# Performance work log

Measured on AMD Instinct MI355X. Metric: run time of the kernel, lower is better.

Reference implementation:

```python
import jax, jax.numpy as jnp
import numpy as np

B, L, F, P = 128, 256, 4, 4   # dialogs, dialog length, future/past links
IN, H, C = 1024, 256, 7
N = B * L


def _build_edges():
    # same structure as build_intra_graph: self-loop + F future + P past per node
    i = np.arange(L)
    ss, tt = [], []
    for d in range(-P, F + 1):
        j = i + d
        m = (j >= 0) & (j < L)
        ss.append(i[m]); tt.append(j[m])
    s = np.concatenate(ss); t = np.concatenate(tt)
    offs = (np.arange(B) * L)[:, None]
    S = (s[None, :] + offs).ravel()
    T = (t[None, :] + offs).ravel()
    return np.stack([S, T]).astype(np.int32)


def setup_inputs() -> dict:
    key = jax.random.key(0)
    ks = jax.random.split(key, 16)
    ei = _build_edges()
    speakers = np.asarray(jax.random.randint(ks[0], (N,), 0, 2), dtype=np.int32)
    rel = (speakers[ei[0]] * speakers[ei[1]]).astype(np.int32)
    sd_in = 1.0 / np.sqrt(IN)
    sd_h = 1.0 / np.sqrt(H)
    return {
        "input": jax.random.normal(ks[1], (N, IN), jnp.float32),
        "dialog_lengths": jnp.full((B,), L, jnp.int32),
        "speakers": jnp.asarray(speakers),
        "labels": jax.random.randint(ks[2], (N,), 0, C, jnp.int32),
        "edge_index": jnp.asarray(ei),
        "rel_type": jnp.asarray(rel),
        # RGCNConv(IN, H, num_relations=2): per-relation weight, root weight, bias
        "W_rgcn": jax.random.normal(ks[3], (2, IN, H), jnp.float32) * sd_in,
        "W_root": jax.random.normal(ks[4], (IN, H), jnp.float32) * sd_in,
        "b_rgcn": jax.random.normal(ks[5], (H,), jnp.float32) * 0.01,
        # GraphConv(H, H): lin_rel (on aggregated neighbors, with bias), lin_root (no bias)
        "W_rel": jax.random.normal(ks[6], (H, H), jnp.float32) * sd_h,
        "b_rel": jax.random.normal(ks[7], (H,), jnp.float32) * 0.01,
        "W_grt": jax.random.normal(ks[8], (H, H), jnp.float32) * sd_h,
        # skip_con: Linear(IN, H)
        "W_skip": jax.random.normal(ks[9], (IN, H), jnp.float32) * sd_in,
        "b_skip": jax.random.normal(ks[10], (H,), jnp.float32) * 0.01,
        # classify: Linear(H, C)
        "W_cls": jax.random.normal(ks[11], (H, C), jnp.float32) * sd_h,
        "b_cls": jax.random.normal(ks[12], (C,), jnp.float32) * 0.01,
    }


def reference(input, dialog_lengths, speakers, labels, edge_index, rel_type,
              W_rgcn, W_root, b_rgcn, W_rel, b_rel, W_grt,
              W_skip, b_skip, W_cls, b_cls):
    n = input.shape[0]
    src, dst = edge_index[0], edge_index[1]
    seg = jax.ops.segment_sum

    # --- RGCNConv: out_i = x_i @ W_root + b + sum_r mean_{j in N_r(i)} x_j @ W_r
    t = jnp.einsum('ni,rio->rno', input, W_rgcn)      # [2, N, H]
    msg = t[rel_type, src]                            # [E, H] relation-specific messages
    h = input @ W_root + b_rgcn
    for r in range(2):
        m = (rel_type == r).astype(input.dtype)       # [E]
        s = seg(msg * m[:, None], dst, num_segments=n)
        cnt = seg(m, dst, num_segments=n)
        h = h + s / jnp.maximum(cnt, 1.0)[:, None]    # mean aggregation per relation

    # --- GraphConv (aggr='add'): out_i = W_rel @ sum_j h_j + b_rel + W_grt @ h_i
    neigh = seg(h[src], dst, num_segments=n)          # [N, H]
    h2 = neigh @ W_rel + b_rel + h @ W_grt

    # --- skip connection + classifier
    out = (h2 + input @ W_skip + b_skip) @ W_cls + b_cls  # [N, C]

    # --- cross entropy (mean)
    logp = jax.nn.log_softmax(out, axis=-1)
    loss = -jnp.mean(jnp.take_along_axis(logp, labels[:, None].astype(jnp.int32), axis=1))
    return out, loss
```

## Files before the change

### kernel.cpp

```cpp
#include <hip/hip_runtime.h>

#define NN 32768
#define INF 1024
#define HF 256

typedef __bf16 bf16x8 __attribute__((ext_vector_type(8)));
typedef float f32x4 __attribute__((ext_vector_type(4)));
typedef unsigned short u16x8 __attribute__((ext_vector_type(8)));

__device__ __forceinline__ float bf2f(unsigned short u) {
  union { unsigned int i; float f; } v; v.i = ((unsigned int)u) << 16; return v.f;
}
__device__ __forceinline__ unsigned short f2bf(float f) {
  union { float f; unsigned int i; } v; v.f = f;
  unsigned int x = v.i;
  return (unsigned short)((x + 0x7fffu + ((x >> 16) & 1u)) >> 16);
}

__device__ __forceinline__ void ld_lds16(const unsigned short* g, unsigned short* l) {
  __builtin_amdgcn_global_load_lds(
      (__attribute__((address_space(1))) const unsigned int*)g,
      (__attribute__((address_space(3))) unsigned int*)l, 16, 0, 0);
}

__global__ __launch_bounds__(256)
void diagcn_prep(const float* __restrict__ x, const float* __restrict__ Wrgcn,
                 const float* __restrict__ Wroot, const float* __restrict__ Wskip,
                 const float* __restrict__ Wgrt, const float* __restrict__ Wrel,
                 unsigned short* __restrict__ Xbf, unsigned short* __restrict__ WbigT,
                 unsigned short* __restrict__ WsmT, float* __restrict__ loss) {
  int bid = blockIdx.x;
  if (bid < 32768) {
    if (bid == 0 && threadIdx.x == 0) loss[0] = 0.f;
    int idx = bid * 256 + threadIdx.x;
    float4 v = ((const float4*)x)[idx];
    ushort4 u; u.x = f2bf(v.x); u.y = f2bf(v.y); u.z = f2bf(v.z); u.w = f2bf(v.w);
    ((ushort4*)Xbf)[idx] = u;
    return;
  }
  __shared__ float tile[64 * 65];
  int tb = bid - 32768;
  const float* src;
  int k0, ncol0;
  unsigned short* dst;
  int ldd, nrow0;
  if (tb < 256) {
    int tn = tb >> 4, tk = tb & 15;
    int mat = tn >> 2;
    src = (mat == 0) ? Wrgcn : (mat == 1) ? (Wrgcn + 262144) : (mat == 2) ? Wroot : Wskip;
    k0 = tk * 64; ncol0 = (tn & 3) * 64;
    dst = WbigT; ldd = 1024; nrow0 = tn * 64;
  } else {
    int t2 = tb - 256;
    int tn = t2 >> 3, tk = t2 & 7;
    src = (tk < 4) ? Wgrt : Wrel;
    k0 = (tk & 3) * 64; ncol0 = tn * 64;
    dst = WsmT; ldd = 512; nrow0 = tn * 64;
  }
  int kdst0 = (tb < 256) ? k0 : (((tb - 256) & 7) * 64);
  int c = threadIdx.x & 63, rb = threadIdx.x >> 6;
#pragma unroll
  for (int it = 0; it < 16; ++it) {
    int r = rb + it * 4;
    tile[r * 65 + c] = src[(size_t)(k0 + r) * 256 + ncol0 + c];
  }
  __syncthreads();
  int kk = threadIdx.x & 63;
#pragma unroll
  for (int it = 0; it < 16; ++it) {
    int nn = rb + it * 4;
    dst[(size_t)(nrow0 + nn) * ldd + kdst0 + kk] = f2bf(tile[kk * 65 + nn]);
  }
}

__global__ __launch_bounds__(256)
void diagcn_gemm1(const unsigned short* __restrict__ A, const unsigned short* __restrict__ BT,
                  unsigned short* __restrict__ Y) {
  const int K = 1024;
  __shared__ unsigned short As[128 * 64];
  __shared__ unsigned short Bs[128 * 64];
  const int tid = threadIdx.x;
  const int w = tid >> 6, lane = tid & 63;
  const int wm = w >> 1, wn = w & 1;
  const int quad = lane >> 4, l15 = lane & 15;
  const int b = blockIdx.x;
  const int m0 = (((b & 7) << 5) + (b >> 6)) << 7;
  const int n0 = ((b >> 3) & 7) << 7;
  const int rowg = lane >> 3;
  const int kbsw = (lane & 7) ^ rowg;

  f32x4 acc[4][4] = {};
  const unsigned short* Abase = A + (size_t)m0 * K + kbsw * 8;
  const unsigned short* Bbase = BT + (size_t)n0 * K + kbsw * 8;

  for (int k0 = 0; k0 < K; k0 += 64) {
#pragma unroll
    for (int t = 0; t < 4; ++t) {
      int grp = w * 4 + t;
      int rl = grp * 8 + rowg;
      ld_lds16(Abase + (size_t)rl * K + k0, &As[grp * 512]);
      ld_lds16(Bbase + (size_t)rl * K + k0, &Bs[grp * 512]);
    }
    __syncthreads();
#pragma unroll
    for (int ks = 0; ks < 2; ++ks) {
      bf16x8 av[4], bv[4];
      int kb = ks * 4 + quad;
#pragma unroll
      for (int i = 0; i < 4; ++i) {
        int ra = wm * 64 + i * 16 + l15;
        int rb2 = wn * 64 + i * 16 + l15;
        av[i] = *(const bf16x8*)&As[ra * 64 + ((kb ^ (ra & 7)) << 3)];
        bv[i] = *(const bf16x8*)&Bs[rb2 * 64 + ((kb ^ (rb2 & 7)) << 3)];
      }
#pragma unroll
      for (int i = 0; i < 4; ++i)
#pragma unroll
        for (int j = 0; j < 4; ++j)
          acc[i][j] = __builtin_amdgcn_mfma_f32_16x16x32_bf16(av[i], bv[j], acc[i][j], 0, 0, 0);
    }
    __syncthreads();
  }
#pragma unroll
  for (int i = 0; i < 4; ++i)
#pragma unroll
    for (int j = 0; j < 4; ++j) {
      int row = m0 + wm * 64 + i * 16 + quad * 4;
      int col = n0 + wn * 64 + j * 16 + l15;
#pragma unroll
      for (int r = 0; r < 4; ++r)
        Y[(size_t)(row + r) * 1024 + col] = f2bf(acc[i][j][r]);
    }
}

__global__ __launch_bounds__(256)
void diagcn_h(const unsigned short* __restrict__ Y, const int* __restrict__ spk,
              const float* __restrict__ brgcn, unsigned short* __restrict__ A2) {
  int b = blockIdx.x;
  int wv = threadIdx.x >> 6, lane = threadIdx.x & 63;
  int half = lane >> 5, li = lane & 31, c0 = li << 3;
  int node = ((b & 7) << 12) + ((b >> 3) << 3) + wv * 2 + half;
  int p = node & 255, dbase = node - p;
  int si = spk[node];
  float a0[8] = {}, a1[8] = {};
  float n0 = 0.f, n1 = 0.f;
#pragma unroll
  for (int d = -4; d <= 4; ++d) {
    int pj = p + d;
    float w = (pj >= 0 && pj < 256) ? 1.f : 0.f;
    int jc = pj < 0 ? 0 : (pj > 255 ? 255 : pj);
    int nj = dbase + jc;
    int rel = si & spk[nj];
    u16x8 v = *(const u16x8*)&Y[(size_t)nj * 1024 + (rel << 8) + c0];
    float w1 = rel ? w : 0.f, w0 = rel ? 0.f : w;
#pragma unroll
    for (int k = 0; k < 8; ++k) {
      float f = bf2f(v[k]);
      a0[k] += f * w0; a1[k] += f * w1;
    }
    n0 += w0; n1 += w1;
  }
  u16x8 vr = *(const u16x8*)&Y[(size_t)node * 1024 + 512 + c0];
  float i0 = 1.f / fmaxf(n0, 1.f), i1 = 1.f / fmaxf(n1, 1.f);
  u16x8 u;
#pragma unroll
  for (int k = 0; k < 8; ++k)
    u[k] = f2bf(bf2f(vr[k]) + brgcn[c0 + k] + a0[k] * i0 + a1[k] * i1);
  *(u16x8*)&A2[(size_t)node * 512 + c0] = u;
}

__global__ __launch_bounds__(256)
void diagcn_neigh(unsigned short* __restrict__ A2) {
  int b = blockIdx.x;
  int wv = threadIdx.x >> 6, lane = threadIdx.x & 63;
  int half = lane >> 5, li = lane & 31, c0 = li << 3;
  int node = ((b & 7) << 12) + ((b >> 3) << 3) + wv * 2 + half;
  int p = node & 255, dbase = node - p;
  float s[8] = {};
#pragma unroll
  for (int d = -4; d <= 4; ++d) {
    int pj = p + d;
    float w = (pj >= 0 && pj < 256) ? 1.f : 0.f;
    int jc = pj < 0 ? 0 : (pj > 255 ? 255 : pj);
    u16x8 v = *(const u16x8*)&A2[(size_t)(dbase + jc) * 512 + c0];
#pragma unroll
    for (int k = 0; k < 8; ++k) s[k] += bf2f(v[k]) * w;
  }
  u16x8 u;
#pragma unroll
  for (int k = 0; k < 8; ++k) u[k] = f2bf(s[k]);
  *(u16x8*)&A2[(size_t)node * 512 + 256 + c0] = u;
}

__global__ __launch_bounds__(256)
void diagcn_gemm2(const unsigned short* __restrict__ A, const unsigned short* __restrict__ BT,
                  const unsigned short* __restrict__ Y, const float* __restrict__ Wcls,
                  const float* __restrict__ bcls, const float* __restrict__ brel,
                  const float* __restrict__ bskip, const int* __restrict__ labels,
                  float* __restrict__ out, float* __restrict__ loss) {
  const int K = 512;
  __shared__ unsigned short As[64 * 64];
  __shared__ unsigned short Bs[256 * 64];
  __shared__ float Wc[2312];
  for (int i = threadIdx.x; i < 2312; i += 256) {
    float v;
    if (i < 1792) v = Wcls[i];
    else if (i < 1799) v = bcls[i - 1792];
    else if (i < 1800) v = 0.f;
    else if (i < 2056) v = brel[i - 1800];
    else v = bskip[i - 2056];
    Wc[i] = v;
  }
  const int tid = threadIdx.x;
  const int w = tid >> 6, lane = tid & 63;
  const int quad = lane >> 4, l15 = lane & 15;
  const int b = blockIdx.x;
  const int m0 = (((b & 7) << 6) + (b >> 3)) << 6;
  const int rowg = lane >> 3;
  const int kbsw = (lane & 7) ^ rowg;

  f32x4 acc[16] = {};
  const unsigned short* Abase = A + (size_t)m0 * K + kbsw * 8;
  const unsigned short* Bbase = BT + kbsw * 8;

  for (int k0 = 0; k0 < K; k0 += 64) {
#pragma unroll
    for (int t = 0; t < 2; ++t) {
      int grp = w * 2 + t;
      ld_lds16(Abase + (size_t)(grp * 8 + rowg) * K + k0, &As[grp * 512]);
    }
#pragma unroll
    for (int t = 0; t < 8; ++t) {
      int grp = w * 8 + t;
      ld_lds16(Bbase + (size_t)(grp * 8 + rowg) * K + k0, &Bs[grp * 512]);
    }
    __syncthreads();
#pragma unroll
    for (int ks = 0; ks < 2; ++ks) {
      int kb = ks * 4 + quad;
      int ra = w * 16 + l15;
      bf16x8 av = *(const bf16x8*)&As[ra * 64 + ((kb ^ (ra & 7)) << 3)];
#pragma unroll
      for (int j = 0; j < 16; ++j) {
        int rb2 = j * 16 + l15;
        bf16x8 bv = *(const bf16x8*)&Bs[rb2 * 64 + ((kb ^ (rb2 & 7)) << 3)];
        acc[j] = __builtin_amdgcn_mfma_f32_16x16x32_bf16(av, bv, acc[j], 0, 0, 0);
      }
    }
    __syncthreads();
  }

  float wsum[4][7] = {};
#pragma unroll
  for (int j = 0; j < 16; ++j) {
    int col = j * 16 + l15;
    float bb = Wc[1800 + col] + Wc[2056 + col];
#pragma unroll
    for (int r = 0; r < 4; ++r) {
      int row = m0 + w * 16 + quad * 4 + r;
      float z = acc[j][r] + bb + bf2f(Y[(size_t)row * 1024 + 768 + col]);
#pragma unroll
      for (int c = 0; c < 7; ++c) wsum[r][c] += z * Wc[col * 7 + c];
    }
  }
#pragma unroll
  for (int o = 1; o < 16; o <<= 1)
#pragma unroll
    for (int r = 0; r < 4; ++r)
#pragma unroll
      for (int c = 0; c < 7; ++c) wsum[r][c] += __shfl_xor(wsum[r][c], o, 64);

  float lsum = 0.f;
#pragma unroll
  for (int r = 0; r < 4; ++r) {
    int row = m0 + w * 16 + quad * 4 + r;
    float o7[7], mx = -1e30f;
#pragma unroll
    for (int c = 0; c < 7; ++c) {
      o7[c] = wsum[r][c] + Wc[1792 + c];
      mx = fmaxf(mx, o7[c]);
    }
    if (l15 < 7) out[(size_t)row * 7 + l15] = o7[l15];
    float s = 0.f;
#pragma unroll
    for (int c = 0; c < 7; ++c) s += expf(o7[c] - mx);
    int lab = labels[row];
    lsum += mx + logf(s) - o7[lab];
  }
  lsum += __shfl_xor(lsum, 16, 64);
  lsum += __shfl_xor(lsum, 32, 64);
  if (lane == 0) atomicAdd(loss, lsum * (1.0f / (float)NN));
}

extern "C" void kernel_launch(void* const* d_in, const int* in_sizes, int n_in,
                              void* d_out, int out_size, void* d_ws, size_t ws_size,
                              hipStream_t stream) {
  const float* x      = (const float*)d_in[0];
  const int* speakers = (const int*)d_in[2];
  const int* labels   = (const int*)d_in[3];
  const float* Wrgcn  = (const float*)d_in[6];
  const float* Wroot  = (const float*)d_in[7];
  const float* brgcn  = (const float*)d_in[8];
  const float* Wrel   = (const float*)d_in[9];
  const float* brel   = (const float*)d_in[10];
  const float* Wgrt   = (const float*)d_in[11];
  const float* Wskip  = (const float*)d_in[12];
  const float* bskip  = (const float*)d_in[13];
  const float* Wcls   = (const float*)d_in[14];
  const float* bcls   = (const float*)d_in[15];
  float* out = (float*)d_out;
  float* loss = out + (size_t)NN * 7;

  const size_t OFF_XBF  = 0;
  const size_t OFF_WBIG = 67108864;
  const size_t OFF_WSM  = 69206016;
  const size_t OFF_Y    = 69468160;
  const size_t OFF_A2   = 136577024;
  const size_t NEED     = 170131456;
  if (ws_size < NEED) return;

  char* ws = (char*)d_ws;
  unsigned short* Xbf   = (unsigned short*)(ws + OFF_XBF);
  unsigned short* WbigT = (unsigned short*)(ws + OFF_WBIG);
  unsigned short* WsmT  = (unsigned short*)(ws + OFF_WSM);
  unsigned short* Y     = (unsigned short*)(ws + OFF_Y);
  unsigned short* A2    = (unsigned short*)(ws + OFF_A2);

  diagcn_prep<<<dim3(33056), dim3(256), 0, stream>>>(x, Wrgcn, Wroot, Wskip, Wgrt, Wrel,
                                                     Xbf, WbigT, WsmT, loss);
  diagcn_gemm1<<<dim3(2048), dim3(256), 0, stream>>>(Xbf, WbigT, Y);
  diagcn_h<<<dim3(NN / 8), dim3(256), 0, stream>>>(Y, speakers, brgcn, A2);
  diagcn_neigh<<<dim3(NN / 8), dim3(256), 0, stream>>>(A2);
  diagcn_gemm2<<<dim3(512), dim3(256), 0, stream>>>(A2, WsmT, Y, Wcls, bcls, brel, bskip,
                                                    labels, out, loss);
}
```

Before: 381.2 us.

## Fuse neighbor aggregation into gemm2 and grid-stride the input conversion

The separate neighbor-sum kernel is removed. gemm2 now computes each 64-row tile's 9-neighbor window sum of H into swizzled LDS, and uses that as the second K half while reading H directly from global memory for the first half. This removes one launch and the A2 write/read round trip, and shrinks the workspace. The prep kernel's fp32-to-bf16 conversion now uses 2048 blocks that each handle 16 strided chunks, instead of one block per chunk. In exchange, gemm2 holds a 32KB tile in LDS, does redundant halo reads, and loads B in smaller K=32 steps with a barrier per step.

```diff
diff --git a/kernel.cpp b/kernel.cpp
--- a/kernel.cpp
+++ b/kernel.cpp
@@ -30,16 +30,21 @@
                  unsigned short* __restrict__ Xbf, unsigned short* __restrict__ WbigT,
                  unsigned short* __restrict__ WsmT, float* __restrict__ loss) {
   int bid = blockIdx.x;
-  if (bid < 32768) {
-    if (bid == 0 && threadIdx.x == 0) loss[0] = 0.f;
-    int idx = bid * 256 + threadIdx.x;
-    float4 v = ((const float4*)x)[idx];
-    ushort4 u; u.x = f2bf(v.x); u.y = f2bf(v.y); u.z = f2bf(v.z); u.w = f2bf(v.w);
-    ((ushort4*)Xbf)[idx] = u;
+  if (bid >= 288) {
+    if (bid == 288 && threadIdx.x == 0) loss[0] = 0.f;
+    int idx = (bid - 288) * 256 + threadIdx.x;
+    const int total = NN * INF / 4;
+    const int stride = 2048 * 256;
+#pragma unroll
+    for (int it = 0; it < 16; ++it, idx += stride) {
+      float4 v = ((const float4*)x)[idx];
+      ushort4 u; u.x = f2bf(v.x); u.y = f2bf(v.y); u.z = f2bf(v.z); u.w = f2bf(v.w);
+      ((ushort4*)Xbf)[idx] = u;
+    }
     return;
   }
   __shared__ float tile[64 * 65];
-  int tb = bid - 32768;
+  int tb = bid;
   const float* src;
   int k0, ncol0;
   unsigned short* dst;
@@ -135,7 +140,7 @@
 
 __global__ __launch_bounds__(256)
 void diagcn_h(const unsigned short* __restrict__ Y, const int* __restrict__ spk,
-              const float* __restrict__ brgcn, unsigned short* __restrict__ A2) {
+              const float* __restrict__ brgcn, unsigned short* __restrict__ H) {
   int b = blockIdx.x;
   int wv = threadIdx.x >> 6, lane = threadIdx.x & 63;
   int half = lane >> 5, li = lane & 31, c0 = li << 3;
@@ -166,43 +171,25 @@
 #pragma unroll
   for (int k = 0; k < 8; ++k)
     u[k] = f2bf(bf2f(vr[k]) + brgcn[c0 + k] + a0[k] * i0 + a1[k] * i1);
-  *(u16x8*)&A2[(size_t)node * 512 + c0] = u;
+  *(u16x8*)&H[(size_t)node * 256 + c0] = u;
 }
 
 __global__ __launch_bounds__(256)
-void diagcn_neigh(unsigned short* __restrict__ A2) {
-  int b = blockIdx.x;
-  int wv = threadIdx.x >> 6, lane = threadIdx.x & 63;
-  int half = lane >> 5, li = lane & 31, c0 = li << 3;
-  int node = ((b & 7) << 12) + ((b >> 3) << 3) + wv * 2 + half;
-  int p = node & 255, dbase = node - p;
-  float s[8] = {};
-#pragma unroll
-  for (int d = -4; d <= 4; ++d) {
-    int pj = p + d;
-    float w = (pj >= 0 && pj < 256) ? 1.f : 0.f;
-    int jc = pj < 0 ? 0 : (pj > 255 ? 255 : pj);
-    u16x8 v = *(const u16x8*)&A2[(size_t)(dbase + jc) * 512 + c0];
-#pragma unroll
-    for (int k = 0; k < 8; ++k) s[k] += bf2f(v[k]) * w;
-  }
-  u16x8 u;
-#pragma unroll
-  for (int k = 0; k < 8; ++k) u[k] = f2bf(s[k]);
-  *(u16x8*)&A2[(size_t)node * 512 + 256 + c0] = u;
-}
-
-__global__ __launch_bounds__(256)
-void diagcn_gemm2(const unsigned short* __restrict__ A, const unsigned short* __restrict__ BT,
+void diagcn_gemm2(const unsigned short* __restrict__ H, const unsigned short* __restrict__ BT,
                   const unsigned short* __restrict__ Y, const float* __restrict__ Wcls,
                   const float* __restrict__ bcls, const float* __restrict__ brel,
                   const float* __restrict__ bskip, const int* __restrict__ labels,
                   float* __restrict__ out, float* __restrict__ loss) {
-  const int K = 512;
-  __shared__ unsigned short As[64 * 64];
-  __shared__ unsigned short Bs[256 * 64];
+  __shared__ unsigned short ns[64 * 256];
+  __shared__ unsigned short Bs[256 * 32];
   __shared__ float Wc[2312];
-  for (int i = threadIdx.x; i < 2312; i += 256) {
+  const int tid = threadIdx.x;
+  const int w = tid >> 6, lane = tid & 63;
+  const int quad = lane >> 4, l15 = lane & 15;
+  const int b = blockIdx.x;
+  const int m0 = (((b & 7) << 6) + (b >> 3)) << 6;
+
+  for (int i = tid; i < 2312; i += 256) {
     float v;
     if (i < 1792) v = Wcls[i];
     else if (i < 1799) v = bcls[i - 1792];
@@ -211,41 +198,55 @@
     else v = bskip[i - 2056];
     Wc[i] = v;
   }
-  const int tid = threadIdx.x;
-  const int w = tid >> 6, lane = tid & 63;
-  const int quad = lane >> 4, l15 = lane & 15;
-  const int b = blockIdx.x;
-  const int m0 = (((b & 7) << 6) + (b >> 3)) << 6;
-  const int rowg = lane >> 3;
-  const int kbsw = (lane & 7) ^ rowg;
-
+
+#pragma unroll
+  for (int it = 0; it < 8; ++it) {
+    int u = tid + it * 256;
+    int t = u >> 5, kb = u & 31;
+    int p = (m0 + t) & 255;
+    float s[8] = {};
+#pragma unroll
+    for (int d = -4; d <= 4; ++d) {
+      int pj = p + d;
+      float wgt = (pj >= 0 && pj < 256) ? 1.f : 0.f;
+      int row = m0 + t + d;
+      row = row < 0 ? 0 : (row > NN - 1 ? NN - 1 : row);
+      u16x8 v = *(const u16x8*)&H[(size_t)row * 256 + kb * 8];
+#pragma unroll
+      for (int k = 0; k < 8; ++k) s[k] += bf2f(v[k]) * wgt;
+    }
+    u16x8 uo;
+#pragma unroll
+    for (int k = 0; k < 8; ++k) uo[k] = f2bf(s[k]);
+    *(u16x8*)&ns[t * 256 + ((kb ^ (t & 7)) << 3)] = uo;
+  }
+  const int srow = lane >> 2;
+  const int sj = lane & 3;
   f32x4 acc[16] = {};
-  const unsigned short* Abase = A + (size_t)m0 * K + kbsw * 8;
-  const unsigned short* Bbase = BT + kbsw * 8;
-
-  for (int k0 = 0; k0 < K; k0 += 64) {
-#pragma unroll
-    for (int t = 0; t < 2; ++t) {
-      int grp = w * 2 + t;
-      ld_lds16(Abase + (size_t)(grp * 8 + rowg) * K + k0, &As[grp * 512]);
-    }
-#pragma unroll
-    for (int t = 0; t < 8; ++t) {
-      int grp = w * 8 + t;
-      ld_lds16(Bbase + (size_t)(grp * 8 + rowg) * K + k0, &Bs[grp * 512]);
+  __syncthreads();
+
+  for (int k0s = 0; k0s < 16; ++k0s) {
+#pragma unroll
+    for (int ps = 0; ps < 4; ++ps) {
+      int pp = w * 4 + ps;
+      int row = pp * 16 + srow;
+      ld_lds16(BT + (size_t)row * 512 + k0s * 32 + ((sj ^ (row & 3)) << 3), &Bs[pp * 512]);
+    }
+    bf16x8 av;
+    if (k0s < 8) {
+      int row = m0 + w * 16 + l15;
+      av = *(const bf16x8*)&H[(size_t)row * 256 + k0s * 32 + quad * 8];
+    } else {
+      int r = w * 16 + l15;
+      int kb = (k0s - 8) * 4 + quad;
+      av = *(const bf16x8*)&ns[r * 256 + ((kb ^ (r & 7)) << 3)];
     }
     __syncthreads();
 #pragma unroll
-    for (int ks = 0; ks < 2; ++ks) {
-      int kb = ks * 4 + quad;
-      int ra = w * 16 + l15;
-      bf16x8 av = *(const bf16x8*)&As[ra * 64 + ((kb ^ (ra & 7)) << 3)];
-#pragma unroll
-      for (int j = 0; j < 16; ++j) {
-        int rb2 = j * 16 + l15;
-        bf16x8 bv = *(const bf16x8*)&Bs[rb2 * 64 + ((kb ^ (rb2 & 7)) << 3)];
-        acc[j] = __builtin_amdgcn_mfma_f32_16x16x32_bf16(av, bv, acc[j], 0, 0, 0);
-      }
+    for (int j = 0; j < 16; ++j) {
+      int rb2 = j * 16 + l15;
+      bf16x8 bv = *(const bf16x8*)&Bs[rb2 * 32 + ((quad ^ (rb2 & 3)) << 3)];
+      acc[j] = __builtin_amdgcn_mfma_f32_16x16x32_bf16(av, bv, acc[j], 0, 0, 0);
     }
     __syncthreads();
   }
@@ -315,8 +316,8 @@
   const size_t OFF_WBIG = 67108864;
   const size_t OFF_WSM  = 69206016;
   const size_t OFF_Y    = 69468160;
-  const size_t OFF_A2   = 136577024;
-  const size_t NEED     = 170131456;
+  const size_t OFF_H    = 136577024;
+  const size_t NEED     = 153354240;
   if (ws_size < NEED) return;
 
   char* ws = (char*)d_ws;
@@ -324,13 +325,12 @@
   unsigned short* WbigT = (unsigned short*)(ws + OFF_WBIG);
   unsigned short* WsmT  = (unsigned short*)(ws + OFF_WSM);
   unsigned short* Y     = (unsigned short*)(ws + OFF_Y);
-  unsigned short* A2    = (unsigned short*)(ws + OFF_A2);
-
-  diagcn_prep<<<dim3(33056), dim3(256), 0, stream>>>(x, Wrgcn, Wroot, Wskip, Wgrt, Wrel,
-                                                     Xbf, WbigT, WsmT, loss);
+  unsigned short* H     = (unsigned short*)(ws + OFF_H);
+
+  diagcn_prep<<<dim3(2336), dim3(256), 0, stream>>>(x, Wrgcn, Wroot, Wskip, Wgrt, Wrel,
+                                                    Xbf, WbigT, WsmT, loss);
   diagcn_gemm1<<<dim3(2048), dim3(256), 0, stream>>>(Xbf, WbigT, Y);
-  diagcn_h<<<dim3(NN / 8), dim3(256), 0, stream>>>(Y, speakers, brgcn, A2);
-  diagcn_neigh<<<dim3(NN / 8), dim3(256), 0, stream>>>(A2);
-  diagcn_gemm2<<<dim3(512), dim3(256), 0, stream>>>(A2, WsmT, Y, Wcls, bcls, brel, bskip,
+  diagcn_h<<<dim3(NN / 8), dim3(256), 0, stream>>>(Y, speakers, brgcn, H);
+  diagcn_gemm2<<<dim3(512), dim3(256), 0, stream>>>(H, WsmT, Y, Wcls, bcls, brel, bskip,
                                                     labels, out, loss);
 }
```

Result: slower. 393.8 us (+3.3%).

## Fuse RGCN aggregation and neighbor sum with LDS halo; coarsen prep conversion

Applied to the files above, without the earlier changes.

Merges the two aggregation kernels into one. Each block computes h for 16 nodes plus a 4-node halo on each side into LDS, then sums neighbors from LDS, which saves a kernel launch and the re-read of A2 from global memory at the cost of recomputing halo rows. The prep kernel's fp32-to-bf16 conversion now runs 16 float4 per thread instead of using tens of thousands of tiny blocks. gemm2 also stages the skip-connection Y slice into LDS with async loads instead of issuing scattered global reads in the epilogue.

```diff
diff --git a/kernel.cpp b/kernel.cpp
--- a/kernel.cpp
+++ b/kernel.cpp
@@ -30,16 +30,20 @@
                  unsigned short* __restrict__ Xbf, unsigned short* __restrict__ WbigT,
                  unsigned short* __restrict__ WsmT, float* __restrict__ loss) {
   int bid = blockIdx.x;
-  if (bid < 32768) {
-    if (bid == 0 && threadIdx.x == 0) loss[0] = 0.f;
-    int idx = bid * 256 + threadIdx.x;
-    float4 v = ((const float4*)x)[idx];
-    ushort4 u; u.x = f2bf(v.x); u.y = f2bf(v.y); u.z = f2bf(v.z); u.w = f2bf(v.w);
-    ((ushort4*)Xbf)[idx] = u;
+  if (bid >= 288) {
+    if (bid == 288 && threadIdx.x == 0) loss[0] = 0.f;
+    int idx = (bid - 288) * 256 + threadIdx.x;
+    const int stride = 2048 * 256;
+#pragma unroll
+    for (int it = 0; it < 16; ++it, idx += stride) {
+      float4 v = ((const float4*)x)[idx];
+      ushort4 u; u.x = f2bf(v.x); u.y = f2bf(v.y); u.z = f2bf(v.z); u.w = f2bf(v.w);
+      ((ushort4*)Xbf)[idx] = u;
+    }
     return;
   }
   __shared__ float tile[64 * 65];
-  int tb = bid - 32768;
+  int tb = bid;
   const float* src;
   int k0, ncol0;
   unsigned short* dst;
@@ -134,62 +138,69 @@
 }
 
 __global__ __launch_bounds__(256)
-void diagcn_h(const unsigned short* __restrict__ Y, const int* __restrict__ spk,
-              const float* __restrict__ brgcn, unsigned short* __restrict__ A2) {
-  int b = blockIdx.x;
-  int wv = threadIdx.x >> 6, lane = threadIdx.x & 63;
-  int half = lane >> 5, li = lane & 31, c0 = li << 3;
-  int node = ((b & 7) << 12) + ((b >> 3) << 3) + wv * 2 + half;
-  int p = node & 255, dbase = node - p;
-  int si = spk[node];
-  float a0[8] = {}, a1[8] = {};
-  float n0 = 0.f, n1 = 0.f;
-#pragma unroll
-  for (int d = -4; d <= 4; ++d) {
-    int pj = p + d;
-    float w = (pj >= 0 && pj < 256) ? 1.f : 0.f;
-    int jc = pj < 0 ? 0 : (pj > 255 ? 255 : pj);
-    int nj = dbase + jc;
-    int rel = si & spk[nj];
-    u16x8 v = *(const u16x8*)&Y[(size_t)nj * 1024 + (rel << 8) + c0];
-    float w1 = rel ? w : 0.f, w0 = rel ? 0.f : w;
-#pragma unroll
-    for (int k = 0; k < 8; ++k) {
-      float f = bf2f(v[k]);
-      a0[k] += f * w0; a1[k] += f * w1;
-    }
-    n0 += w0; n1 += w1;
-  }
-  u16x8 vr = *(const u16x8*)&Y[(size_t)node * 1024 + 512 + c0];
-  float i0 = 1.f / fmaxf(n0, 1.f), i1 = 1.f / fmaxf(n1, 1.f);
-  u16x8 u;
-#pragma unroll
-  for (int k = 0; k < 8; ++k)
-    u[k] = f2bf(bf2f(vr[k]) + brgcn[c0 + k] + a0[k] * i0 + a1[k] * i1);
-  *(u16x8*)&A2[(size_t)node * 512 + c0] = u;
-}
-
-__global__ __launch_bounds__(256)
-void diagcn_neigh(unsigned short* __restrict__ A2) {
-  int b = blockIdx.x;
-  int wv = threadIdx.x >> 6, lane = threadIdx.x & 63;
-  int half = lane >> 5, li = lane & 31, c0 = li << 3;
-  int node = ((b & 7) << 12) + ((b >> 3) << 3) + wv * 2 + half;
-  int p = node & 255, dbase = node - p;
-  float s[8] = {};
-#pragma unroll
-  for (int d = -4; d <= 4; ++d) {
-    int pj = p + d;
-    float w = (pj >= 0 && pj < 256) ? 1.f : 0.f;
-    int jc = pj < 0 ? 0 : (pj > 255 ? 255 : pj);
-    u16x8 v = *(const u16x8*)&A2[(size_t)(dbase + jc) * 512 + c0];
-#pragma unroll
-    for (int k = 0; k < 8; ++k) s[k] += bf2f(v[k]) * w;
-  }
-  u16x8 u;
-#pragma unroll
-  for (int k = 0; k < 8; ++k) u[k] = f2bf(s[k]);
-  *(u16x8*)&A2[(size_t)node * 512 + 256 + c0] = u;
+void diagcn_hn(const unsigned short* __restrict__ Y, const int* __restrict__ spk,
+               const float* __restrict__ brgcn, unsigned short* __restrict__ A2) {
+  __shared__ unsigned short hl[24 * 256];
+  const int b = blockIdx.x;
+  const int nb = ((b & 7) << 12) + ((b >> 3) << 4);
+  const int p0 = nb & 255, dbase = nb - p0;
+  const int tid = threadIdx.x;
+#pragma unroll
+  for (int it = 0; it < 3; ++it) {
+    int u = tid + it * 256;
+    int r = u >> 5, cb = u & 31, c0 = cb << 3;
+    int p = p0 - 4 + r;
+    int pc = p < 0 ? 0 : (p > 255 ? 255 : p);
+    int node = dbase + pc;
+    int si = spk[node];
+    float a0[8] = {}, a1[8] = {};
+    float n0 = 0.f, n1 = 0.f;
+#pragma unroll
+    for (int d = -4; d <= 4; ++d) {
+      int pj = p + d;
+      float w = (pj >= 0 && pj < 256) ? 1.f : 0.f;
+      int jc = pj < 0 ? 0 : (pj > 255 ? 255 : pj);
+      int nj = dbase + jc;
+      int rel = si & spk[nj];
+      u16x8 v = *(const u16x8*)&Y[(size_t)nj * 1024 + (rel << 8) + c0];
+      float w1 = rel ? w : 0.f, w0 = rel ? 0.f : w;
+#pragma unroll
+      for (int k = 0; k < 8; ++k) {
+        float f = bf2f(v[k]);
+        a0[k] += f * w0; a1[k] += f * w1;
+      }
+      n0 += w0; n1 += w1;
+    }
+    u16x8 vr = *(const u16x8*)&Y[(size_t)node * 1024 + 512 + c0];
+    float i0 = 1.f / fmaxf(n0, 1.f), i1 = 1.f / fmaxf(n1, 1.f);
+    u16x8 uo;
+#pragma unroll
+    for (int k = 0; k < 8; ++k)
+      uo[k] = f2bf(bf2f(vr[k]) + brgcn[c0 + k] + a0[k] * i0 + a1[k] * i1);
+    *(u16x8*)&hl[r * 256 + c0] = uo;
+    if (r >= 4 && r < 20)
+      *(u16x8*)&A2[(size_t)(dbase + p) * 512 + c0] = uo;
+  }
+  __syncthreads();
+#pragma unroll
+  for (int it = 0; it < 2; ++it) {
+    int u = tid + it * 256;
+    int r = u >> 5, cb = u & 31, c0 = cb << 3;
+    int p = p0 + r;
+    float s[8] = {};
+#pragma unroll
+    for (int d = -4; d <= 4; ++d) {
+      int pj = p + d;
+      float w = (pj >= 0 && pj < 256) ? 1.f : 0.f;
+      u16x8 v = *(const u16x8*)&hl[(r + 4 + d) * 256 + c0];
+#pragma unroll
+      for (int k = 0; k < 8; ++k) s[k] += bf2f(v[k]) * w;
+    }
+    u16x8 uo;
+#pragma unroll
+    for (int k = 0; k < 8; ++k) uo[k] = f2bf(s[k]);
+    *(u16x8*)&A2[(size_t)(nb + r) * 512 + 256 + c0] = uo;
+  }
 }
 
 __global__ __launch_bounds__(256)
@@ -250,6 +261,16 @@
     __syncthreads();
   }
 
+  unsigned short* Ysk = Bs;
+  {
+    int row2 = w * 2 + (lane >> 5);
+    const unsigned short* ysrc = Y + (size_t)(m0 + row2) * 1024 + 768 + (lane & 31) * 8;
+#pragma unroll
+    for (int pS = 0; pS < 8; ++pS)
+      ld_lds16(ysrc + (size_t)pS * 8 * 1024, &Ysk[(pS * 8 + w * 2) * 256]);
+  }
+  __syncthreads();
+
   float wsum[4][7] = {};
 #pragma unroll
   for (int j = 0; j < 16; ++j) {
@@ -257,8 +278,8 @@
     float bb = Wc[1800 + col] + Wc[2056 + col];
 #pragma unroll
     for (int r = 0; r < 4; ++r) {
-      int row = m0 + w * 16 + quad * 4 + r;
-      float z = acc[j][r] + bb + bf2f(Y[(size_t)row * 1024 + 768 + col]);
+      int lrow = w * 16 + quad * 4 + r;
+      float z = acc[j][r] + bb + bf2f(Ysk[lrow * 256 + col]);
 #pragma unroll
       for (int c = 0; c < 7; ++c) wsum[r][c] += z * Wc[col * 7 + c];
     }
@@ -326,11 +347,10 @@
   unsigned short* Y     = (unsigned short*)(ws + OFF_Y);
   unsigned short* A2    = (unsigned short*)(ws + OFF_A2);
 
-  diagcn_prep<<<dim3(33056), dim3(256), 0, stream>>>(x, Wrgcn, Wroot, Wskip, Wgrt, Wrel,
-                                                     Xbf, WbigT, WsmT, loss);
+  diagcn_prep<<<dim3(2336), dim3(256), 0, stream>>>(x, Wrgcn, Wroot, Wskip, Wgrt, Wrel,
+                                                    Xbf, WbigT, WsmT, loss);
   diagcn_gemm1<<<dim3(2048), dim3(256), 0, stream>>>(Xbf, WbigT, Y);
-  diagcn_h<<<dim3(NN / 8), dim3(256), 0, stream>>>(Y, speakers, brgcn, A2);
-  diagcn_neigh<<<dim3(NN / 8), dim3(256), 0, stream>>>(A2);
+  diagcn_hn<<<dim3(2048), dim3(256), 0, stream>>>(Y, speakers, brgcn, A2);
   diagcn_gemm2<<<dim3(512), dim3(256), 0, stream>>>(A2, WsmT, Y, Wcls, bcls, brel, bskip,
                                                     labels, out, loss);
 }
```

Result: slower. 394.2 us (+3.4%).
